# Optimization experiments

Hardware: AMD Instinct MI355X
Metric: run time of the kernel (lower is better)

The kernel has to match this reference:

```python
import jax, jax.numpy as jnp
import numpy as np
import math

B, S, D, H, L, F = 32, 512, 512, 8, 4, 2048
DK = D // H
EPS = 1e-5


def _cosine_pos_emb(seq_len, d_model):
    pe = np.zeros((seq_len, d_model), dtype=np.float32)
    position = np.arange(seq_len, dtype=np.float32)[:, None]
    div_term = np.exp(np.arange(0, d_model, 2, dtype=np.float32) * (-math.log(10000.0) / d_model))
    pe[:, 0::2] = np.sin(position * div_term)
    pe[:, 1::2] = np.cos(position * div_term)
    return jnp.asarray(pe[None])  # (1, S, D)


def setup_inputs() -> dict:
    key = jax.random.key(0)
    ks = jax.random.split(key, 12)
    w = 0.02
    return {
        "q_embed_data": jax.random.normal(ks[0], (B, S, D), jnp.float32),
        "qa_embed_data": jax.random.normal(ks[1], (B, S, D), jnp.float32),
        "forget_rate": jax.random.uniform(ks[2], (B, S, 1), jnp.float32),
        "pos_emb": _cosine_pos_emb(S, D),
        # per-layer stacked params (torch Linear convention: W is (out,in))
        "Wk": w * jax.random.normal(ks[3], (L, D, D), jnp.float32),
        "bk": jnp.zeros((L, D), jnp.float32),
        "Wv": w * jax.random.normal(ks[4], (L, D, D), jnp.float32),
        "bv": jnp.zeros((L, D), jnp.float32),
        "Wo": w * jax.random.normal(ks[5], (L, D, D), jnp.float32),
        "bo": jnp.zeros((L, D), jnp.float32),
        "W1": w * jax.random.normal(ks[6], (L, F, D), jnp.float32),
        "b1": jnp.zeros((L, F), jnp.float32),
        "W2": w * jax.random.normal(ks[7], (L, D, F), jnp.float32),
        "b2": jnp.zeros((L, D), jnp.float32),
        "ln1_g": jnp.ones((L, D), jnp.float32),
        "ln1_b": jnp.zeros((L, D), jnp.float32),
        "ln2_g": jnp.ones((L, D), jnp.float32),
        "ln2_b": jnp.zeros((L, D), jnp.float32),
    }


def _layer_norm(x, g, b):
    mu = jnp.mean(x, axis=-1, keepdims=True)
    var = jnp.mean(jnp.square(x - mu), axis=-1, keepdims=True)
    return (x - mu) * jax.lax.rsqrt(var + EPS) * g + b


def _forward(q_embed_data, qa_embed_data, forget_rate, pos_emb,
             Wk, bk, Wv, bv, Wo, bo, W1, b1, W2, b2,
             ln1_g, ln1_b, ln2_g, ln2_b):
    x = q_embed_data + pos_emb   # queries/keys stream
    y = qa_embed_data + pos_emb  # values stream (fixed across layers)
    scale = 1.0 / math.sqrt(DK)
    # mask=0 path: triu(k=0)==0 -> strictly past positions only (j < i)
    allowed = jnp.tril(jnp.ones((S, S), dtype=bool), k=-1)
    fr = forget_rate[:, None, :, :]  # (B,1,S,1): row-wise decay on scores
    neg = jnp.asarray(-1e32, x.dtype)

    def block(x, p):
        wk, bk_, wv, bv_, wo, bo_, w1, b1_, w2, b2_, g1, be1, g2, be2 = p
        # kq_same=1: q and k share the k_linear projection (so q == k here)
        kq = (jnp.einsum('bsd,ed->bse', x, wk) + bk_).reshape(B, S, H, DK).transpose(0, 2, 1, 3)
        v = (jnp.einsum('bsd,ed->bse', y, wv) + bv_).reshape(B, S, H, DK).transpose(0, 2, 1, 3)
        scores = jnp.einsum('bhsd,bhtd->bhst', kq, kq) * scale
        scores = scores * fr
        scores = jnp.where(allowed, scores, neg)
        attn = jax.nn.softmax(scores, axis=-1)
        attn = attn.at[:, :, 0, :].set(0.0)  # zero_pad: first query row zeroed
        ctx = jnp.einsum('bhst,bhtd->bhsd', attn, v).transpose(0, 2, 1, 3).reshape(B, S, D)
        out = jnp.einsum('bsd,ed->bse', ctx, wo) + bo_
        x = _layer_norm(x + out, g1, be1)
        ff = jnp.einsum('bsf,df->bsd', jax.nn.relu(jnp.einsum('bsd,fd->bsf', x, w1) + b1_), w2) + b2_
        x = _layer_norm(x + ff, g2, be2)
        return x, None

    x, _ = jax.lax.scan(block, x, (Wk, bk, Wv, bv, Wo, bo, W1, b1, W2, b2, ln1_g, ln1_b, ln2_g, ln2_b))
    return x


def reference(q_embed_data, qa_embed_data, forget_rate, pos_emb,
              Wk, bk, Wv, bv, Wo, bo, W1, b1, W2, b2,
              ln1_g, ln1_b, ln2_g, ln2_b):
    return _forward(q_embed_data, qa_embed_data, forget_rate, pos_emb,
                    Wk, bk, Wv, bv, Wo, bo, W1, b1, W2, b2,
                    ln1_g, ln1_b, ln2_g, ln2_b)
```

## Files before the change

kernel.cpp:

```cpp
#include <hip/hip_runtime.h>
#include <hip/hip_bf16.h>

constexpr int B_ = 32, S_ = 512, D_ = 512, H_ = 8, L_ = 4, F_ = 2048, DK_ = 64;

typedef __attribute__((ext_vector_type(8))) short short8;
typedef __attribute__((ext_vector_type(4))) float f32x4;

__device__ inline unsigned short f2b(float f) {
  union { __hip_bfloat16 h; unsigned short u; } cv;
  cv.h = __float2bfloat16(f);
  return cv.u;
}
__device__ inline float b2f(unsigned short u) {
  union { unsigned int i; float f; } c;
  c.i = ((unsigned int)u) << 16;
  return c.f;
}
__device__ inline float waveReduceSum(float v) {
  #pragma unroll
  for (int o = 32; o > 0; o >>= 1) v += __shfl_xor(v, o);
  return v;
}

__global__ void prep_kernel(const float4* __restrict__ q, const float4* __restrict__ qa,
                            const float4* __restrict__ pos, float4* __restrict__ xf,
                            uint2* __restrict__ xb, uint2* __restrict__ yb) {
  int i = blockIdx.x * blockDim.x + threadIdx.x;
  float4 p = pos[i & 65535];
  float4 a = q[i], c = qa[i];
  float4 xv, yv;
  xv.x = a.x + p.x; xv.y = a.y + p.y; xv.z = a.z + p.z; xv.w = a.w + p.w;
  yv.x = c.x + p.x; yv.y = c.y + p.y; yv.z = c.z + p.z; yv.w = c.w + p.w;
  xf[i] = xv;
  uint2 px, py;
  px.x = (unsigned)f2b(xv.x) | ((unsigned)f2b(xv.y) << 16);
  px.y = (unsigned)f2b(xv.z) | ((unsigned)f2b(xv.w) << 16);
  py.x = (unsigned)f2b(yv.x) | ((unsigned)f2b(yv.y) << 16);
  py.y = (unsigned)f2b(yv.z) | ((unsigned)f2b(yv.w) << 16);
  xb[i] = px;
  yb[i] = py;
}

__global__ void cast_kernel(const float4* __restrict__ src, uint2* __restrict__ dst, int n4) {
  int i = blockIdx.x * blockDim.x + threadIdx.x;
  if (i >= n4) return;
  float4 v = src[i];
  uint2 p;
  p.x = (unsigned)f2b(v.x) | ((unsigned)f2b(v.y) << 16);
  p.y = (unsigned)f2b(v.z) | ((unsigned)f2b(v.w) << 16);
  dst[i] = p;
}

template<int RELU, int STORE>
__global__ __launch_bounds__(256, 2) void gemm128_kernel(
    const __hip_bfloat16* __restrict__ A,
    const __hip_bfloat16* __restrict__ W,
    const float* __restrict__ bias,
    const __hip_bfloat16* __restrict__ A2,
    const __hip_bfloat16* __restrict__ W2,
    const float* __restrict__ bias2,
    __hip_bfloat16* __restrict__ Cb,
    __hip_bfloat16* __restrict__ Cb2,
    int Ndim, int Kdim, int kLen)
{
  __shared__ char lds[32768];
  const int tid = threadIdx.x, wave = tid >> 6, lane = tid & 63;
  const int rl = lane & 15, gq = lane >> 4;
  const int wr = wave >> 1, wc = wave & 1;

  const int nwg = gridDim.x * gridDim.y;
  const int lin = blockIdx.y * gridDim.x + blockIdx.x;
  const int swz = (lin & 7) * (nwg >> 3) + (lin >> 3);
  const int bx = swz % gridDim.x, by = swz / gridDim.x;

  const int row0 = by * 128;
  const int col0 = bx * 128;

  const __hip_bfloat16* Ap = A;
  const __hip_bfloat16* Wp = W;
  const float* bp = bias;
  int kOff = blockIdx.z * kLen;
  if (STORE == 3) {
    kOff = 0;
    if (blockIdx.z) { Ap = A2; Wp = W2; bp = bias2; }
  }

  f32x4 acc[4][4] = {};
  const int ntiles = kLen >> 5;

  auto stage = [&](int kt, int d) {
    const int kbase = kOff + (kt << 5);
    #pragma unroll
    for (int r = 0; r < 2; ++r) {
      int p = r * 4096 + tid * 16;
      int R = p >> 6, c = (p >> 4) & 3;
      int gc = c ^ ((R >> 1) & 3);
      const __hip_bfloat16* srcA = Ap + (size_t)(row0 + R) * Kdim + kbase + gc * 8;
      __builtin_amdgcn_global_load_lds(
          (const __attribute__((address_space(1))) void*)srcA,
          (__attribute__((address_space(3))) void*)(lds + d * 8192 + p), 16, 0, 0);
      const __hip_bfloat16* srcW = Wp + (size_t)(col0 + R) * Kdim + kbase + gc * 8;
      __builtin_amdgcn_global_load_lds(
          (const __attribute__((address_space(1))) void*)srcW,
          (__attribute__((address_space(3))) void*)(lds + 16384 + d * 8192 + p), 16, 0, 0);
    }
  };

  stage(0, 0);
  __syncthreads();
  for (int kt = 0; kt < ntiles; ++kt) {
    const int d = kt & 1;
    if (kt + 1 < ntiles) stage(kt + 1, d ^ 1);

    short8 aF[4], bF[4];
    #pragma unroll
    for (int m = 0; m < 4; ++m) {
      int rr = wr * 64 + m * 16 + rl;
      aF[m] = *(const short8*)(lds + d * 8192 + rr * 64 + ((gq ^ ((rr >> 1) & 3)) << 4));
    }
    #pragma unroll
    for (int n = 0; n < 4; ++n) {
      int rr = wc * 64 + n * 16 + rl;
      bF[n] = *(const short8*)(lds + 16384 + d * 8192 + rr * 64 + ((gq ^ ((rr >> 1) & 3)) << 4));
    }
    __builtin_amdgcn_s_setprio(1);
    #pragma unroll
    for (int m = 0; m < 4; ++m)
      #pragma unroll
      for (int n = 0; n < 4; ++n)
        acc[m][n] = __builtin_amdgcn_mfma_f32_16x16x32_bf16(aF[m], bF[n], acc[m][n], 0, 0, 0);
    __builtin_amdgcn_s_setprio(0);
    __syncthreads();
  }

  char* sw = lds + wave * 8192;
  const bool vt = (STORE == 3) && (blockIdx.z == 1);
  const bool addb = (STORE == 3) ? true : ((bias != nullptr) && (blockIdx.z == 0));
  float bvv[4];
  #pragma unroll
  for (int n = 0; n < 4; ++n)
    bvv[n] = addb ? bp[col0 + wc * 64 + n * 16 + rl] : 0.0f;

  #pragma unroll
  for (int n = 0; n < 4; ++n)
    #pragma unroll
    for (int m = 0; m < 4; ++m)
      #pragma unroll
      for (int j = 0; j < 4; ++j) {
        float val = acc[m][n][j] + bvv[n];
        if (RELU) val = fmaxf(val, 0.0f);
        int addr;
        if (vt) {
          int orow = n * 16 + rl, ocol = m * 16 + gq * 4 + j;
          addr = orow * 128 + ((ocol * 2) ^ ((orow & 7) << 4));
        } else {
          int orow = m * 16 + gq * 4 + j;
          addr = orow * 128 + (((n * 16 + rl) * 2) ^ (((orow >> 1) & 7) << 4));
        }
        *(unsigned short*)(sw + addr) = f2b(val);
      }
  asm volatile("s_waitcnt lgkmcnt(0)" ::: "memory");
  __builtin_amdgcn_sched_barrier(0);

  __hip_bfloat16* Cbd = blockIdx.z ? Cb2 : Cb;
  const int cchunk = lane & 7;
  if (vt) {
    const int bh64 = ((row0 >> 9) * 8 + (col0 >> 6) + wc) * 64;
    const int tbase = (row0 & 511) + wr * 64;
    #pragma unroll
    for (int it = 0; it < 8; ++it) {
      int d0 = it * 8 + (lane >> 3);
      uint4 vv = *(const uint4*)(sw + d0 * 128 + ((cchunk * 16) ^ ((d0 & 7) << 4)));
      *(uint4*)((char*)Cbd + ((size_t)(bh64 + d0) * 512 + tbase) * 2 + cchunk * 16) = vv;
    }
  } else {
    #pragma unroll
    for (int it = 0; it < 8; ++it) {
      int orow = it * 8 + (lane >> 3);
      uint4 vv = *(const uint4*)(sw + orow * 128 + ((cchunk * 16) ^ (((orow >> 1) & 7) << 4)));
      *(uint4*)((char*)Cbd + ((size_t)(row0 + wr * 64 + orow) * Ndim + col0 + wc * 64) * 2 +
                cchunk * 16) = vv;
    }
  }
}

__global__ __launch_bounds__(512, 2) void fattn_kernel(
    const __hip_bfloat16* __restrict__ kq,
    const __hip_bfloat16* __restrict__ vT,
    const float* __restrict__ fr,
    __hip_bfloat16* __restrict__ ctx)
{
  __shared__ char lds[147456];
  const int tid = threadIdx.x, wave = tid >> 6, lane = tid & 63;
  const int rl = lane & 15, gq = lane >> 4;
  const int bh = blockIdx.x & 255;
  const int blk = blockIdx.x >> 8;
  const int b = bh >> 3, h = bh & 7;
  const size_t kqbase = ((size_t)b * S_) * D_ + h * DK_;
  const size_t vtbase = ((size_t)bh * DK_) * S_;
  const char* kg = (const char*)kq + kqbase * 2;
  const char* vg = (const char*)vT + vtbase * 2;

  #pragma unroll
  for (int i = 0; i < 8; ++i) {
    int p = i * 8192 + tid * 16;
    int r = p >> 7, ch = (p >> 4) & 7;
    __builtin_amdgcn_global_load_lds(
        (const __attribute__((address_space(1))) void*)(kg + (size_t)r * 1024 + ((ch ^ (r & 7)) << 4)),
        (__attribute__((address_space(3))) void*)(lds + p), 16, 0, 0);
  }
  #pragma unroll
  for (int i = 0; i < 8; ++i) {
    int p = i * 8192 + tid * 16;
    int d = p >> 10, ck = (p >> 4) & 63;
    __builtin_amdgcn_global_load_lds(
        (const __attribute__((address_space(1))) void*)(vg + (size_t)d * 1024 + ((ck ^ (d & 7)) << 4)),
        (__attribute__((address_space(3))) void*)(lds + 65536 + p), 16, 0, 0);
  }

  const int qidx = blk * 8 + (wave < 4 ? wave : 11 - wave);
  const int qw0 = qidx * 32;
  const int nt = (qidx >> 1) + 1;

  float sfv[2][4];
  #pragma unroll
  for (int qf = 0; qf < 2; ++qf)
    #pragma unroll
    for (int j = 0; j < 4; ++j)
      sfv[qf][j] = fr[b * S_ + qw0 + qf * 16 + gq * 4 + j] * 0.125f;

  asm volatile("s_waitcnt vmcnt(0)" ::: "memory");
  __builtin_amdgcn_sched_barrier(0);
  __builtin_amdgcn_s_barrier();

  short8 qA[2][2];
  #pragma unroll
  for (int qf = 0; qf < 2; ++qf)
    #pragma unroll
    for (int kf = 0; kf < 2; ++kf) {
      int r = qw0 + qf * 16 + rl;
      qA[qf][kf] = *(const short8*)(lds + r * 128 + (((kf * 4 + gq) ^ (r & 7)) << 4));
    }

  f32x4 o[2][4] = {};
  float mrow[2][4], lrow[2][4];
  #pragma unroll
  for (int qf = 0; qf < 2; ++qf)
    #pragma unroll
    for (int j = 0; j < 4; ++j) { mrow[qf][j] = -3.0e38f; lrow[qf][j] = 0.0f; }

  char* pbase = lds + 131072 + wave * 2048;

  for (int ti = 0; ti < nt; ++ti) {
    const int t0 = ti << 6;
    short8 kB[4][2];
    #pragma unroll
    for (int tf = 0; tf < 4; ++tf)
      #pragma unroll
      for (int kf = 0; kf < 2; ++kf) {
        int r = t0 + tf * 16 + rl;
        kB[tf][kf] = *(const short8*)(lds + r * 128 + (((kf * 4 + gq) ^ (r & 7)) << 4));
      }
    short8 vB[4][2];
    #pragma unroll
    for (int df = 0; df < 4; ++df)
      #pragma unroll
      for (int kf = 0; kf < 2; ++kf) {
        int d = df * 16 + rl;
        vB[df][kf] = *(const short8*)(lds + 65536 + d * 1024 +
                                      ((8 * ti + ((kf * 4 + gq) ^ (d & 7))) << 4));
      }

    #pragma unroll
    for (int qf = 0; qf < 2; ++qf) {
      f32x4 c4[4] = {};
      #pragma unroll
      for (int tf = 0; tf < 4; ++tf)
        #pragma unroll
        for (int kf = 0; kf < 2; ++kf)
          c4[tf] = __builtin_amdgcn_mfma_f32_16x16x32_bf16(qA[qf][kf], kB[tf][kf], c4[tf], 0, 0, 0);

      const int qg0 = qw0 + qf * 16 + gq * 4;
      #pragma unroll
      for (int tf = 0; tf < 4; ++tf) {
        int tg = t0 + tf * 16 + rl;
        #pragma unroll
        for (int j = 0; j < 4; ++j) {
          float s = c4[tf][j] * sfv[qf][j];
          c4[tf][j] = (tg >= qg0 + j) ? -3.0e38f : s;
        }
      }
      float tm[4];
      #pragma unroll
      for (int j = 0; j < 4; ++j) {
        tm[j] = fmaxf(fmaxf(c4[0][j], c4[1][j]), fmaxf(c4[2][j], c4[3][j]));
        #pragma unroll
        for (int msk = 1; msk < 16; msk <<= 1) tm[j] = fmaxf(tm[j], __shfl_xor(tm[j], msk));
      }
      #pragma unroll
      for (int j = 0; j < 4; ++j) {
        float mn = fmaxf(mrow[qf][j], tm[j]);
        float fac = __expf(mrow[qf][j] - mn);
        mrow[qf][j] = mn;
        lrow[qf][j] *= fac;
        #pragma unroll
        for (int df = 0; df < 4; ++df) o[qf][df][j] *= fac;
      }
      float rs[4] = {0.f, 0.f, 0.f, 0.f};
      #pragma unroll
      for (int tf = 0; tf < 4; ++tf) {
        int tloc = tf * 16 + rl;
        #pragma unroll
        for (int j = 0; j < 4; ++j) {
          float e = __expf(c4[tf][j] - mrow[qf][j]);
          rs[j] += e;
          int qloc = gq * 4 + j;
          int addr = qloc * 128 + ((((tloc >> 3) ^ (qloc & 7)) << 4)) + (tloc & 7) * 2;
          *(unsigned short*)(pbase + addr) = f2b(e);
        }
      }
      #pragma unroll
      for (int j = 0; j < 4; ++j) {
        float r = rs[j];
        #pragma unroll
        for (int msk = 1; msk < 16; msk <<= 1) r += __shfl_xor(r, msk);
        lrow[qf][j] += r;
      }
      asm volatile("s_waitcnt lgkmcnt(0)" ::: "memory");
      __builtin_amdgcn_sched_barrier(0);
      short8 pA[2];
      #pragma unroll
      for (int kf = 0; kf < 2; ++kf)
        pA[kf] = *(const short8*)(pbase + rl * 128 + (((kf * 4 + gq) ^ (rl & 7)) << 4));
      #pragma unroll
      for (int df = 0; df < 4; ++df)
        #pragma unroll
        for (int kf = 0; kf < 2; ++kf)
          o[qf][df] = __builtin_amdgcn_mfma_f32_16x16x32_bf16(pA[kf], vB[df][kf], o[qf][df], 0, 0, 0);
    }
  }

  #pragma unroll
  for (int qf = 0; qf < 2; ++qf)
    #pragma unroll
    for (int j = 0; j < 4; ++j) {
      int qg = qw0 + qf * 16 + gq * 4 + j;
      float inv = (qg == 0) ? 0.0f : 1.0f / lrow[qf][j];
      #pragma unroll
      for (int df = 0; df < 4; ++df) {
        union { __hip_bfloat16 hh; unsigned short u; } cv;
        cv.u = f2b(o[qf][df][j] * inv);
        ctx[((size_t)(b * S_ + qg)) * D_ + h * DK_ + df * 16 + rl] = cv.hh;
      }
    }
}

template<int NADD>
__global__ __launch_bounds__(256) void ln_kernel(
    const float4* __restrict__ xin, const uint4* __restrict__ add,
    const uint4* __restrict__ add2,
    const float* __restrict__ g, const float* __restrict__ bta,
    float4* xf_out, uint2* __restrict__ xb_out)
{
  const int lane = threadIdx.x & 63, wv = threadIdx.x >> 6;
  const size_t row = (size_t)blockIdx.x * 4 + wv;
  const size_t base4 = row * 128;

  float4 x0 = xin[base4 + lane * 2], x1 = xin[base4 + lane * 2 + 1];
  uint4 ab = add[row * 64 + lane];
  const unsigned short* ap = (const unsigned short*)&ab;
  float v[8];
  v[0] = x0.x; v[1] = x0.y; v[2] = x0.z; v[3] = x0.w;
  v[4] = x1.x; v[5] = x1.y; v[6] = x1.z; v[7] = x1.w;
  #pragma unroll
  for (int i = 0; i < 8; ++i) v[i] += b2f(ap[i]);
  if (NADD == 2) {
    uint4 ab2 = add2[row * 64 + lane];
    const unsigned short* ap2 = (const unsigned short*)&ab2;
    #pragma unroll
    for (int i = 0; i < 8; ++i) v[i] += b2f(ap2[i]);
  }
  float s = 0.0f;
  #pragma unroll
  for (int i = 0; i < 8; ++i) s += v[i];
  s = waveReduceSum(s);
  float mu = s * (1.0f / 512.0f);
  float vs = 0.0f;
  #pragma unroll
  for (int i = 0; i < 8; ++i) { float dd = v[i] - mu; vs += dd * dd; }
  vs = waveReduceSum(vs);
  float rstd = rsqrtf(vs * (1.0f / 512.0f) + 1e-5f);

  const int c0i = lane * 8;
  float4 gg0 = *(const float4*)(g + c0i), gg1 = *(const float4*)(g + c0i + 4);
  float4 bb0 = *(const float4*)(bta + c0i), bb1 = *(const float4*)(bta + c0i + 4);
  float o[8];
  o[0] = (v[0] - mu) * rstd * gg0.x + bb0.x;
  o[1] = (v[1] - mu) * rstd * gg0.y + bb0.y;
  o[2] = (v[2] - mu) * rstd * gg0.z + bb0.z;
  o[3] = (v[3] - mu) * rstd * gg0.w + bb0.w;
  o[4] = (v[4] - mu) * rstd * gg1.x + bb1.x;
  o[5] = (v[5] - mu) * rstd * gg1.y + bb1.y;
  o[6] = (v[6] - mu) * rstd * gg1.z + bb1.z;
  o[7] = (v[7] - mu) * rstd * gg1.w + bb1.w;
  float4 w0, w1;
  w0.x = o[0]; w0.y = o[1]; w0.z = o[2]; w0.w = o[3];
  w1.x = o[4]; w1.y = o[5]; w1.z = o[6]; w1.w = o[7];
  xf_out[base4 + lane * 2] = w0;
  xf_out[base4 + lane * 2 + 1] = w1;
  uint2 p0, p1;
  p0.x = (unsigned)f2b(o[0]) | ((unsigned)f2b(o[1]) << 16);
  p0.y = (unsigned)f2b(o[2]) | ((unsigned)f2b(o[3]) << 16);
  p1.x = (unsigned)f2b(o[4]) | ((unsigned)f2b(o[5]) << 16);
  p1.y = (unsigned)f2b(o[6]) | ((unsigned)f2b(o[7]) << 16);
  xb_out[row * 128 + lane * 2] = p0;
  xb_out[row * 128 + lane * 2 + 1] = p1;
}

extern "C" void kernel_launch(void* const* d_in, const int* in_sizes, int n_in,
                              void* d_out, int out_size, void* d_ws, size_t ws_size,
                              hipStream_t stream) {
  (void)in_sizes; (void)n_in; (void)out_size; (void)ws_size;
  const float* q   = (const float*)d_in[0];
  const float* qa  = (const float*)d_in[1];
  const float* frr = (const float*)d_in[2];
  const float* pos = (const float*)d_in[3];
  const float* Wk  = (const float*)d_in[4];
  const float* bk  = (const float*)d_in[5];
  const float* Wv  = (const float*)d_in[6];
  const float* bv  = (const float*)d_in[7];
  const float* Wo  = (const float*)d_in[8];
  const float* bo  = (const float*)d_in[9];
  const float* W1  = (const float*)d_in[10];
  const float* b1  = (const float*)d_in[11];
  const float* W2  = (const float*)d_in[12];
  const float* b2  = (const float*)d_in[13];
  const float* g1  = (const float*)d_in[14];
  const float* be1 = (const float*)d_in[15];
  const float* g2  = (const float*)d_in[16];
  const float* be2 = (const float*)d_in[17];

  char* ws = (char*)d_ws;
  float*          xf   = (float*)(ws + 0);
  __hip_bfloat16* xb   = (__hip_bfloat16*)(ws + 33554432);
  __hip_bfloat16* yb   = (__hip_bfloat16*)(ws + 50331648);
  __hip_bfloat16* kqb  = (__hip_bfloat16*)(ws + 67108864);
  __hip_bfloat16* vtb  = (__hip_bfloat16*)(ws + 83886080);
  __hip_bfloat16* ctxb = (__hip_bfloat16*)(ws + 100663296);
  __hip_bfloat16* hb   = (__hip_bfloat16*)(ws + 117440512);
  __hip_bfloat16* wkb  = (__hip_bfloat16*)(ws + 184549376);
  __hip_bfloat16* wvb  = (__hip_bfloat16*)(ws + 186646528);
  __hip_bfloat16* wob  = (__hip_bfloat16*)(ws + 188743680);
  __hip_bfloat16* w1b  = (__hip_bfloat16*)(ws + 190840832);
  __hip_bfloat16* w2b  = (__hip_bfloat16*)(ws + 199229440);
  __hip_bfloat16* obf = (__hip_bfloat16*)(ws + 67108864);
  __hip_bfloat16* pf0 = (__hip_bfloat16*)(ws + 83886080);
  __hip_bfloat16* pf1 = (__hip_bfloat16*)(ws + 100663296);

  prep_kernel<<<8192, 256, 0, stream>>>((const float4*)q, (const float4*)qa,
                                        (const float4*)pos, (float4*)xf,
                                        (uint2*)xb, (uint2*)yb);
  cast_kernel<<<1024, 256, 0, stream>>>((const float4*)Wk, (uint2*)wkb, 262144);
  cast_kernel<<<1024, 256, 0, stream>>>((const float4*)Wv, (uint2*)wvb, 262144);
  cast_kernel<<<1024, 256, 0, stream>>>((const float4*)Wo, (uint2*)wob, 262144);
  cast_kernel<<<4096, 256, 0, stream>>>((const float4*)W1, (uint2*)w1b, 1048576);
  cast_kernel<<<4096, 256, 0, stream>>>((const float4*)W2, (uint2*)w2b, 1048576);

  for (int l = 0; l < L_; ++l) {
    gemm128_kernel<0,3><<<dim3(4, 128, 2), 256, 0, stream>>>(
        xb, wkb + (size_t)l * 262144, bk + l * 512,
        yb, wvb + (size_t)l * 262144, bv + l * 512,
        kqb, vtb, 512, 512, 512);
    fattn_kernel<<<512, 512, 0, stream>>>(kqb, vtb, frr, ctxb);
    gemm128_kernel<0,0><<<dim3(4, 128, 1), 256, 0, stream>>>(
        ctxb, wob + (size_t)l * 262144, bo + l * 512,
        nullptr, nullptr, nullptr, obf, nullptr, 512, 512, 512);
    ln_kernel<1><<<4096, 256, 0, stream>>>((const float4*)xf, (const uint4*)obf, nullptr,
                                           g1 + l * 512, be1 + l * 512,
                                           (float4*)xf, (uint2*)xb);
    gemm128_kernel<1,0><<<dim3(16, 128, 1), 256, 0, stream>>>(
        xb, w1b + (size_t)l * 1048576, b1 + l * 2048,
        nullptr, nullptr, nullptr, hb, nullptr, 2048, 512, 512);
    gemm128_kernel<0,0><<<dim3(4, 128, 2), 256, 0, stream>>>(
        hb, w2b + (size_t)l * 1048576, b2 + l * 512,
        nullptr, nullptr, nullptr, pf0, pf1, 512, 2048, 1024);
    float* lnout = (l == L_ - 1) ? (float*)d_out : xf;
    ln_kernel<2><<<4096, 256, 0, stream>>>((const float4*)xf, (const uint4*)pf0,
                                           (const uint4*)pf1,
                                           g2 + l * 512, be2 + l * 512,
                                           (float4*)lnout, (uint2*)xb);
  }
}
```

Baseline: 854.2 us.

## Rewrite causal attention with 32x32 MFMA and register-only P transpose

The attention kernel now uses one block per (batch, head) instead of two. Each wave handles a balanced pair of query tiles (i and 15-i) with 32x32x16 MFMA, computing S transposed so each lane owns one query row. Softmax probabilities stay in registers: they are packed to bf16 and exchanged across lanes with a cross-half shuffle, which removes the per-wave LDS round trip and its waits. The V swizzle changes to 16-way, and the grid is halved. This means fewer blocks, which risks lower occupancy or less latency hiding.

```diff
diff --git a/kernel.cpp b/kernel.cpp
--- a/kernel.cpp
+++ b/kernel.cpp
@@ -5,6 +5,7 @@
 
 typedef __attribute__((ext_vector_type(8))) short short8;
 typedef __attribute__((ext_vector_type(4))) float f32x4;
+typedef __attribute__((ext_vector_type(16))) float f32x16;
 
 __device__ inline unsigned short f2b(float f) {
   union { __hip_bfloat16 h; unsigned short u; } cv;
@@ -15,6 +16,11 @@
   union { unsigned int i; float f; } c;
   c.i = ((unsigned int)u) << 16;
   return c.f;
+}
+__device__ inline unsigned pkbf(float a, float b) {
+  unsigned r;
+  asm("v_cvt_pk_bf16_f32 %0, %1, %2" : "=v"(r) : "v"(a), "v"(b));
+  return r;
 }
 __device__ inline float waveReduceSum(float v) {
   #pragma unroll
@@ -190,11 +196,10 @@
     const float* __restrict__ fr,
     __hip_bfloat16* __restrict__ ctx)
 {
-  __shared__ char lds[147456];
+  __shared__ char lds[131072];
   const int tid = threadIdx.x, wave = tid >> 6, lane = tid & 63;
-  const int rl = lane & 15, gq = lane >> 4;
-  const int bh = blockIdx.x & 255;
-  const int blk = blockIdx.x >> 8;
+  const int lq = lane & 31, hi = lane >> 5;
+  const int bh = blockIdx.x;
   const int b = bh >> 3, h = bh & 7;
   const size_t kqbase = ((size_t)b * S_) * D_ + h * DK_;
   const size_t vtbase = ((size_t)bh * DK_) * S_;
@@ -204,9 +209,9 @@
   #pragma unroll
   for (int i = 0; i < 8; ++i) {
     int p = i * 8192 + tid * 16;
-    int r = p >> 7, ch = (p >> 4) & 7;
+    int r = p >> 7, ck = (p >> 4) & 7;
     __builtin_amdgcn_global_load_lds(
-        (const __attribute__((address_space(1))) void*)(kg + (size_t)r * 1024 + ((ch ^ (r & 7)) << 4)),
+        (const __attribute__((address_space(1))) void*)(kg + (size_t)r * 1024 + ((ck ^ (r & 7)) << 4)),
         (__attribute__((address_space(3))) void*)(lds + p), 16, 0, 0);
   }
   #pragma unroll
@@ -214,145 +219,123 @@
     int p = i * 8192 + tid * 16;
     int d = p >> 10, ck = (p >> 4) & 63;
     __builtin_amdgcn_global_load_lds(
-        (const __attribute__((address_space(1))) void*)(vg + (size_t)d * 1024 + ((ck ^ (d & 7)) << 4)),
+        (const __attribute__((address_space(1))) void*)(vg + (size_t)d * 1024 + ((ck ^ (d & 15)) << 4)),
         (__attribute__((address_space(3))) void*)(lds + 65536 + p), 16, 0, 0);
   }
 
-  const int qidx = blk * 8 + (wave < 4 ? wave : 11 - wave);
-  const int qw0 = qidx * 32;
-  const int nt = (qidx >> 1) + 1;
-
-  float sfv[2][4];
-  #pragma unroll
-  for (int qf = 0; qf < 2; ++qf)
-    #pragma unroll
-    for (int j = 0; j < 4; ++j)
-      sfv[qf][j] = fr[b * S_ + qw0 + qf * 16 + gq * 4 + j] * 0.125f;
+  const int qia = wave, qib = 15 - wave;
+  const int na = qia + 1, nb = qib + 1;
+  const int sa = qia * 32 + lq, sb = qib * 32 + lq;
+  const float sfa = fr[b * S_ + sa] * 0.125f;
+  const float sfb = fr[b * S_ + sb] * 0.125f;
 
   asm volatile("s_waitcnt vmcnt(0)" ::: "memory");
   __builtin_amdgcn_sched_barrier(0);
   __builtin_amdgcn_s_barrier();
 
-  short8 qA[2][2];
-  #pragma unroll
-  for (int qf = 0; qf < 2; ++qf)
-    #pragma unroll
-    for (int kf = 0; kf < 2; ++kf) {
-      int r = qw0 + qf * 16 + rl;
-      qA[qf][kf] = *(const short8*)(lds + r * 128 + (((kf * 4 + gq) ^ (r & 7)) << 4));
-    }
-
-  f32x4 o[2][4] = {};
-  float mrow[2][4], lrow[2][4];
-  #pragma unroll
-  for (int qf = 0; qf < 2; ++qf)
-    #pragma unroll
-    for (int j = 0; j < 4; ++j) { mrow[qf][j] = -3.0e38f; lrow[qf][j] = 0.0f; }
-
-  char* pbase = lds + 131072 + wave * 2048;
-
-  for (int ti = 0; ti < nt; ++ti) {
-    const int t0 = ti << 6;
-    short8 kB[4][2];
-    #pragma unroll
-    for (int tf = 0; tf < 4; ++tf)
-      #pragma unroll
-      for (int kf = 0; kf < 2; ++kf) {
-        int r = t0 + tf * 16 + rl;
-        kB[tf][kf] = *(const short8*)(lds + r * 128 + (((kf * 4 + gq) ^ (r & 7)) << 4));
-      }
-    short8 vB[4][2];
-    #pragma unroll
-    for (int df = 0; df < 4; ++df)
-      #pragma unroll
-      for (int kf = 0; kf < 2; ++kf) {
-        int d = df * 16 + rl;
-        vB[df][kf] = *(const short8*)(lds + 65536 + d * 1024 +
-                                      ((8 * ti + ((kf * 4 + gq) ^ (d & 7))) << 4));
-      }
-
-    #pragma unroll
-    for (int qf = 0; qf < 2; ++qf) {
-      f32x4 c4[4] = {};
-      #pragma unroll
-      for (int tf = 0; tf < 4; ++tf)
-        #pragma unroll
-        for (int kf = 0; kf < 2; ++kf)
-          c4[tf] = __builtin_amdgcn_mfma_f32_16x16x32_bf16(qA[qf][kf], kB[tf][kf], c4[tf], 0, 0, 0);
-
-      const int qg0 = qw0 + qf * 16 + gq * 4;
-      #pragma unroll
-      for (int tf = 0; tf < 4; ++tf) {
-        int tg = t0 + tf * 16 + rl;
-        #pragma unroll
-        for (int j = 0; j < 4; ++j) {
-          float s = c4[tf][j] * sfv[qf][j];
-          c4[tf][j] = (tg >= qg0 + j) ? -3.0e38f : s;
-        }
-      }
-      float tm[4];
-      #pragma unroll
-      for (int j = 0; j < 4; ++j) {
-        tm[j] = fmaxf(fmaxf(c4[0][j], c4[1][j]), fmaxf(c4[2][j], c4[3][j]));
-        #pragma unroll
-        for (int msk = 1; msk < 16; msk <<= 1) tm[j] = fmaxf(tm[j], __shfl_xor(tm[j], msk));
-      }
-      #pragma unroll
-      for (int j = 0; j < 4; ++j) {
-        float mn = fmaxf(mrow[qf][j], tm[j]);
-        float fac = __expf(mrow[qf][j] - mn);
-        mrow[qf][j] = mn;
-        lrow[qf][j] *= fac;
-        #pragma unroll
-        for (int df = 0; df < 4; ++df) o[qf][df][j] *= fac;
-      }
-      float rs[4] = {0.f, 0.f, 0.f, 0.f};
-      #pragma unroll
-      for (int tf = 0; tf < 4; ++tf) {
-        int tloc = tf * 16 + rl;
-        #pragma unroll
-        for (int j = 0; j < 4; ++j) {
-          float e = __expf(c4[tf][j] - mrow[qf][j]);
-          rs[j] += e;
-          int qloc = gq * 4 + j;
-          int addr = qloc * 128 + ((((tloc >> 3) ^ (qloc & 7)) << 4)) + (tloc & 7) * 2;
-          *(unsigned short*)(pbase + addr) = f2b(e);
-        }
-      }
-      #pragma unroll
-      for (int j = 0; j < 4; ++j) {
-        float r = rs[j];
-        #pragma unroll
-        for (int msk = 1; msk < 16; msk <<= 1) r += __shfl_xor(r, msk);
-        lrow[qf][j] += r;
-      }
-      asm volatile("s_waitcnt lgkmcnt(0)" ::: "memory");
-      __builtin_amdgcn_sched_barrier(0);
-      short8 pA[2];
-      #pragma unroll
-      for (int kf = 0; kf < 2; ++kf)
-        pA[kf] = *(const short8*)(pbase + rl * 128 + (((kf * 4 + gq) ^ (rl & 7)) << 4));
-      #pragma unroll
-      for (int df = 0; df < 4; ++df)
-        #pragma unroll
-        for (int kf = 0; kf < 2; ++kf)
-          o[qf][df] = __builtin_amdgcn_mfma_f32_16x16x32_bf16(pA[kf], vB[df][kf], o[qf][df], 0, 0, 0);
-    }
-  }
-
-  #pragma unroll
-  for (int qf = 0; qf < 2; ++qf)
-    #pragma unroll
-    for (int j = 0; j < 4; ++j) {
-      int qg = qw0 + qf * 16 + gq * 4 + j;
-      float inv = (qg == 0) ? 0.0f : 1.0f / lrow[qf][j];
-      #pragma unroll
-      for (int df = 0; df < 4; ++df) {
-        union { __hip_bfloat16 hh; unsigned short u; } cv;
-        cv.u = f2b(o[qf][df][j] * inv);
-        ctx[((size_t)(b * S_ + qg)) * D_ + h * DK_ + df * 16 + rl] = cv.hh;
-      }
-    }
+  short8 qa_[4], qb_[4];
+  #pragma unroll
+  for (int f = 0; f < 4; ++f) {
+    qa_[f] = *(const short8*)(lds + sa * 128 + ((((f << 1) + hi) ^ (sa & 7)) << 4));
+    qb_[f] = *(const short8*)(lds + sb * 128 + ((((f << 1) + hi) ^ (sb & 7)) << 4));
+  }
+
+  f32x16 oa0 = {}, oa1 = {}, ob0 = {}, ob1 = {};
+  float ma = -3.0e38f, la = 0.0f, mb = -3.0e38f, lb = 0.0f;
+
+  auto process = [&](f32x16& o0, f32x16& o1, float& m, float& l,
+                     const short8* qf, int srow, float sf,
+                     const short8* kb, const short8* vb0, const short8* vb1,
+                     int t0) {
+    f32x16 s = {};
+    #pragma unroll
+    for (int f = 0; f < 4; ++f)
+      s = __builtin_amdgcn_mfma_f32_32x32x16_bf16(kb[f], qf[f], s, 0, 0, 0);
+    float p[16];
+    #pragma unroll
+    for (int r = 0; r < 16; ++r) {
+      int tg = t0 + (r & 3) + 8 * (r >> 2) + 4 * hi;
+      float v = s[r] * sf;
+      p[r] = (tg >= srow) ? -3.0e38f : v;
+    }
+    float t8[8], t4[4];
+    #pragma unroll
+    for (int i = 0; i < 8; ++i) t8[i] = fmaxf(p[2 * i], p[2 * i + 1]);
+    #pragma unroll
+    for (int i = 0; i < 4; ++i) t4[i] = fmaxf(t8[2 * i], t8[2 * i + 1]);
+    float mt = fmaxf(fmaxf(t4[0], t4[1]), fmaxf(t4[2], t4[3]));
+    mt = fmaxf(mt, __shfl_xor(mt, 32));
+    float mn = fmaxf(m, mt);
+    float fac = __expf(m - mn);
+    m = mn;
+    l *= fac;
+    #pragma unroll
+    for (int r = 0; r < 16; ++r) p[r] = __expf(p[r] - mn);
+    float s8[8], s4[4];
+    #pragma unroll
+    for (int i = 0; i < 8; ++i) s8[i] = p[2 * i] + p[2 * i + 1];
+    #pragma unroll
+    for (int i = 0; i < 4; ++i) s4[i] = s8[2 * i] + s8[2 * i + 1];
+    float ps = (s4[0] + s4[1]) + (s4[2] + s4[3]);
+    ps += __shfl_xor(ps, 32);
+    l += ps;
+    #pragma unroll
+    for (int i = 0; i < 16; ++i) { o0[i] *= fac; o1[i] *= fac; }
+    #pragma unroll
+    for (int c = 0; c < 2; ++c) {
+      unsigned X0 = pkbf(p[8 * c + 0], p[8 * c + 1]);
+      unsigned X1 = pkbf(p[8 * c + 2], p[8 * c + 3]);
+      unsigned Y0 = pkbf(p[8 * c + 4], p[8 * c + 5]);
+      unsigned Y1 = pkbf(p[8 * c + 6], p[8 * c + 7]);
+      unsigned z0 = hi ? X0 : Y0, z1 = hi ? X1 : Y1;
+      unsigned r0 = __shfl_xor(z0, 32), r1 = __shfl_xor(z1, 32);
+      union { unsigned u[4]; short8 v; } pb;
+      pb.u[0] = hi ? r0 : X0;
+      pb.u[1] = hi ? r1 : X1;
+      pb.u[2] = hi ? Y0 : r0;
+      pb.u[3] = hi ? Y1 : r1;
+      o0 = __builtin_amdgcn_mfma_f32_32x32x16_bf16(vb0[c], pb.v, o0, 0, 0, 0);
+      o1 = __builtin_amdgcn_mfma_f32_32x32x16_bf16(vb1[c], pb.v, o1, 0, 0, 0);
+    }
+  };
+
+  for (int ti = 0; ti < nb; ++ti) {
+    const int t0 = ti * 32;
+    short8 kb[4];
+    #pragma unroll
+    for (int f = 0; f < 4; ++f) {
+      int tw = t0 + lq;
+      kb[f] = *(const short8*)(lds + tw * 128 + ((((f << 1) + hi) ^ (tw & 7)) << 4));
+    }
+    short8 vb0[2], vb1[2];
+    #pragma unroll
+    for (int c = 0; c < 2; ++c) {
+      int ck = 4 * ti + 2 * c + hi;
+      int d0 = lq;
+      vb0[c] = *(const short8*)(lds + 65536 + d0 * 1024 + ((ck ^ (d0 & 15)) << 4));
+      int d1 = 32 + lq;
+      vb1[c] = *(const short8*)(lds + 65536 + d1 * 1024 + ((ck ^ (d1 & 15)) << 4));
+    }
+    if (ti < na) process(oa0, oa1, ma, la, qa_, sa, sfa, kb, vb0, vb1, t0);
+    process(ob0, ob1, mb, lb, qb_, sb, sfb, kb, vb0, vb1, t0);
+  }
+
+  auto writeO = [&](const f32x16& o0, const f32x16& o1, float l, int srow) {
+    float inv = (srow == 0) ? 0.0f : 1.0f / l;
+    char* base = (char*)ctx + (((size_t)(b * S_ + srow)) * D_ + h * DK_) * 2;
+    #pragma unroll
+    for (int g = 0; g < 4; ++g) {
+      uint2 w0, w1;
+      w0.x = pkbf(o0[4 * g + 0] * inv, o0[4 * g + 1] * inv);
+      w0.y = pkbf(o0[4 * g + 2] * inv, o0[4 * g + 3] * inv);
+      *(uint2*)(base + (8 * g + 4 * hi) * 2) = w0;
+      w1.x = pkbf(o1[4 * g + 0] * inv, o1[4 * g + 1] * inv);
+      w1.y = pkbf(o1[4 * g + 2] * inv, o1[4 * g + 3] * inv);
+      *(uint2*)(base + (32 + 8 * g + 4 * hi) * 2) = w1;
+    }
+  };
+  writeO(oa0, oa1, la, sa);
+  writeO(ob0, ob1, lb, sb);
 }
 
 template<int NADD>
@@ -471,7 +454,7 @@
         xb, wkb + (size_t)l * 262144, bk + l * 512,
         yb, wvb + (size_t)l * 262144, bv + l * 512,
         kqb, vtb, 512, 512, 512);
-    fattn_kernel<<<512, 512, 0, stream>>>(kqb, vtb, frr, ctxb);
+    fattn_kernel<<<256, 512, 0, stream>>>(kqb, vtb, frr, ctxb);
     gemm128_kernel<0,0><<<dim3(4, 128, 1), 256, 0, stream>>>(
         ctxb, wob + (size_t)l * 262144, bo + l * 512,
         nullptr, nullptr, nullptr, obf, nullptr, 512, 512, 512);
```

After: 793.2 us. 7.1% less time.
